# Performance work log

Hardware: AMD Instinct MI355X
Metric: run time of the kernel (lower is better)

## Reference

```python
import jax, jax.numpy as jnp
import numpy as np

B = 16384          # batch
N_SPARSE = 16      # single-id sparse features
N_VARLEN = 4       # variable-length sparse features
L = 50             # max sequence length per varlen feature
V = 1_000_000      # vocab per table
D = 1              # linear embedding dim (DeepCTR Linear uses dim=1)
INIT_STD = 1e-4
EPS = 1e-8


def setup_inputs() -> dict:
    key = jax.random.key(0)
    k1, k2, k3 = jax.random.split(key, 3)
    X = jax.random.randint(k1, (B, N_SPARSE + N_VARLEN * L), 0, V, dtype=jnp.int32)
    sparse_tables = jax.random.normal(k2, (N_SPARSE, V, D), dtype=jnp.float32) * INIT_STD
    varlen_tables = jax.random.normal(k3, (N_VARLEN, V, D), dtype=jnp.float32) * INIT_STD
    return {"X": X, "sparse_tables": sparse_tables, "varlen_tables": varlen_tables}


def reference(X, sparse_tables, varlen_tables):
    # --- single-id sparse lookups: one gather per table, vectorized over tables ---
    sparse_ids = X[:, :N_SPARSE]                                  # [B, Ns]
    f_idx = jnp.arange(N_SPARSE)[None, :]                          # [1, Ns]
    sparse_emb = sparse_tables[f_idx, sparse_ids]                  # [B, Ns, D]

    # --- varlen lookups + masked mean pooling (mask: id != 0, DeepCTR convention) ---
    varlen_ids = X[:, N_SPARSE:].reshape(B, N_VARLEN, L)           # [B, Nv, L]
    v_idx = jnp.arange(N_VARLEN)[None, :, None]                    # [1, Nv, 1]
    varlen_emb = varlen_tables[v_idx, varlen_ids]                  # [B, Nv, L, D]
    mask = (varlen_ids != 0).astype(varlen_emb.dtype)[..., None]   # [B, Nv, L, 1]
    summed = jnp.sum(varlen_emb * mask, axis=2)                    # [B, Nv, D]
    lengths = jnp.sum(mask, axis=2)                                # [B, Nv, 1]
    pooled = summed / (lengths + EPS)                              # [B, Nv, D]

    # --- concat and flatten, matching torch.flatten(concat_fun(...), start_dim=1) ---
    out = jnp.concatenate([sparse_emb, pooled], axis=1)            # [B, Ns+Nv, D]
    return out.reshape(B, -1)                                      # [B, (Ns+Nv)*D]
```

## Files before the change

### kernel.cpp

```cpp
#include <hip/hip_runtime.h>

#define B 16384
#define N_SPARSE 16
#define N_VARLEN 4
#define L 50
#define V 1000000
#define ROW (N_SPARSE + N_VARLEN * L)
#define OUT_W (N_SPARSE + N_VARLEN)
#define KLANES 8

#define VARLEN_BLOCKS 2048
#define SPARSE_BLOCKS 1024
#define NVEC 3
#define NID  7

typedef int v2i __attribute__((ext_vector_type(2)));

__global__ __launch_bounds__(256) void emb_gather_pool_kernel(
    const int* __restrict__ X,
    const float* __restrict__ sparse_tables,
    const float* __restrict__ varlen_tables,
    float* __restrict__ out)
{
    const int bid = blockIdx.x;
    const int t   = threadIdx.x;

    if (bid < VARLEN_BLOCKS) {
        const int xcd  = bid & 7;
        const int f    = xcd & 3;
        const int half = xcd >> 2;
        const int slot = bid >> 3;
        const int task = t >> 3;
        const int lane = t & (KLANES - 1);
        const int row  = half * (B / 2) + slot * 32 + task;

        const int*   ids = X + row * ROW + N_SPARSE + f * L;
        const float* tab = varlen_tables + (long)f * V;

        int id[NID];
        #pragma unroll
        for (int k = 0; k < NVEC; ++k) {
            const v2i w = __builtin_nontemporal_load(
                reinterpret_cast<const v2i*>(ids + 2 * lane + 16 * k));
            id[2 * k]     = w.x;
            id[2 * k + 1] = w.y;
        }
        id[6] = (lane < 2) ? __builtin_nontemporal_load(ids + 48 + lane) : 0;

        float v[NID];
        #pragma unroll
        for (int k = 0; k < 6; ++k) {
            v[k] = tab[id[k]];
        }
        v[6] = 0.0f;
        if (lane < 2) {
            v[6] = tab[id[6]];
        }

        float sum = 0.0f;
        float cnt = 0.0f;
        #pragma unroll
        for (int k = 0; k < NID; ++k) {
            const float m = (id[k] != 0) ? 1.0f : 0.0f;
            sum = fmaf(m, v[k], sum);
            cnt += m;
        }

        #pragma unroll
        for (int off = 1; off < KLANES; off <<= 1) {
            sum += __shfl_xor(sum, off);
            cnt += __shfl_xor(cnt, off);
        }

        if (lane == 0) {
            __builtin_nontemporal_store(sum / (cnt + 1e-8f),
                                        out + row * OUT_W + N_SPARSE + f);
        }
    } else {
        const int sb  = bid - VARLEN_BLOCKS;
        const int rl  = t >> 4;
        const int j   = t & 15;
        const int row = sb * 16 + rl;

        const int   id = __builtin_nontemporal_load(X + row * ROW + j);
        const float v  = __builtin_nontemporal_load(sparse_tables + (long)j * V + id);
        __builtin_nontemporal_store(v, out + row * OUT_W + j);
    }
}

extern "C" void kernel_launch(void* const* d_in, const int* in_sizes, int n_in,
                              void* d_out, int out_size, void* d_ws, size_t ws_size,
                              hipStream_t stream) {
    const int*   X             = (const int*)  d_in[0];
    const float* sparse_tables = (const float*)d_in[1];
    const float* varlen_tables = (const float*)d_in[2];
    float*       out           = (float*)d_out;

    const int grid  = VARLEN_BLOCKS + SPARSE_BLOCKS;
    const int block = 256;

    emb_gather_pool_kernel<<<grid, block, 0, stream>>>(X, sparse_tables, varlen_tables, out);
}
```

Before: 126.5 us.

## Prefetch varlen tables with a streaming warm-up kernel before the gather

Adds a warm_kernel that reads all four varlen embedding tables sequentially with vector loads, so they sit in the large last-level cache before the random gathers run. Its result goes to the workspace scaled near zero, only so the loads are not optimised away. The main kernel is reordered so the sparse-lookup blocks come first and the varlen blocks after, with the per-XCD feature mapping kept. The intent is to turn scattered HBM accesses into cache hits, at the cost of an extra launch and a full 16MB streaming read on every call.

New measurement: 129.4 us. 2.3% more time.

```diff
diff --git a/kernel.cpp b/kernel.cpp
--- a/kernel.cpp
+++ b/kernel.cpp
@@ -9,12 +9,36 @@
 #define OUT_W (N_SPARSE + N_VARLEN)
 #define KLANES 8
 
+#define SPARSE_BLOCKS 1024
 #define VARLEN_BLOCKS 2048
-#define SPARSE_BLOCKS 1024
-#define NVEC 3
-#define NID  7
+#define WARM_BLOCKS   2048
 
-typedef int v2i __attribute__((ext_vector_type(2)));
+typedef int   v2i __attribute__((ext_vector_type(2)));
+typedef float v4f __attribute__((ext_vector_type(4)));
+
+__global__ __launch_bounds__(256) void warm_kernel(
+    const float* __restrict__ varlen_tables,
+    float* __restrict__ ws)
+{
+    const int bid  = blockIdx.x;
+    const int t    = threadIdx.x;
+    const int xcd  = bid & 7;
+    const int f    = xcd & 3;
+    const int slot = bid >> 3;
+    const float* tab = varlen_tables + (long)f * V;
+
+    float acc = 0.0f;
+    const int base = slot * 4096 + t * 4;
+    #pragma unroll
+    for (int c = 0; c < 4; ++c) {
+        const int g = base + c * 1024;
+        if (g + 4 <= V) {
+            const v4f w = *reinterpret_cast<const v4f*>(tab + g);
+            acc += w.x + w.y + w.z + w.w;
+        }
+    }
+    ws[bid] = acc * 1e-30f;
+}
 
 __global__ __launch_bounds__(256) void emb_gather_pool_kernel(
     const int* __restrict__ X,
@@ -25,66 +49,67 @@
     const int bid = blockIdx.x;
     const int t   = threadIdx.x;
 
-    if (bid < VARLEN_BLOCKS) {
-        const int xcd  = bid & 7;
-        const int f    = xcd & 3;
-        const int half = xcd >> 2;
-        const int slot = bid >> 3;
-        const int task = t >> 3;
-        const int lane = t & (KLANES - 1);
-        const int row  = half * (B / 2) + slot * 32 + task;
-
-        const int*   ids = X + row * ROW + N_SPARSE + f * L;
-        const float* tab = varlen_tables + (long)f * V;
-
-        int id[NID];
-        #pragma unroll
-        for (int k = 0; k < NVEC; ++k) {
-            const v2i w = __builtin_nontemporal_load(
-                reinterpret_cast<const v2i*>(ids + 2 * lane + 16 * k));
-            id[2 * k]     = w.x;
-            id[2 * k + 1] = w.y;
-        }
-        id[6] = (lane < 2) ? __builtin_nontemporal_load(ids + 48 + lane) : 0;
-
-        float v[NID];
-        #pragma unroll
-        for (int k = 0; k < 6; ++k) {
-            v[k] = tab[id[k]];
-        }
-        v[6] = 0.0f;
-        if (lane < 2) {
-            v[6] = tab[id[6]];
-        }
-
-        float sum = 0.0f;
-        float cnt = 0.0f;
-        #pragma unroll
-        for (int k = 0; k < NID; ++k) {
-            const float m = (id[k] != 0) ? 1.0f : 0.0f;
-            sum = fmaf(m, v[k], sum);
-            cnt += m;
-        }
-
-        #pragma unroll
-        for (int off = 1; off < KLANES; off <<= 1) {
-            sum += __shfl_xor(sum, off);
-            cnt += __shfl_xor(cnt, off);
-        }
-
-        if (lane == 0) {
-            __builtin_nontemporal_store(sum / (cnt + 1e-8f),
-                                        out + row * OUT_W + N_SPARSE + f);
-        }
-    } else {
-        const int sb  = bid - VARLEN_BLOCKS;
+    if (bid < SPARSE_BLOCKS) {
         const int rl  = t >> 4;
         const int j   = t & 15;
-        const int row = sb * 16 + rl;
+        const int row = bid * 16 + rl;
 
         const int   id = __builtin_nontemporal_load(X + row * ROW + j);
         const float v  = __builtin_nontemporal_load(sparse_tables + (long)j * V + id);
         __builtin_nontemporal_store(v, out + row * OUT_W + j);
+        return;
+    }
+
+    const int vb   = bid - SPARSE_BLOCKS;
+    const int xcd  = bid & 7;
+    const int f    = xcd & 3;
+    const int half = xcd >> 2;
+    const int slot = vb >> 3;
+    const int task = t >> 3;
+    const int lane = t & (KLANES - 1);
+    const int row  = half * (B / 2) + slot * 32 + task;
+
+    const int*   ids = X + row * ROW + N_SPARSE + f * L;
+    const float* tab = varlen_tables + (long)f * V;
+
+    int id[7];
+    #pragma unroll
+    for (int k = 0; k < 3; ++k) {
+        const v2i w = __builtin_nontemporal_load(
+            reinterpret_cast<const v2i*>(ids + 2 * lane + 16 * k));
+        id[2 * k]     = w.x;
+        id[2 * k + 1] = w.y;
+    }
+    id[6] = (lane < 2) ? __builtin_nontemporal_load(ids + 48 + lane) : 0;
+
+    float v[7];
+    #pragma unroll
+    for (int k = 0; k < 6; ++k) {
+        v[k] = tab[id[k]];
+    }
+    v[6] = 0.0f;
+    if (lane < 2) {
+        v[6] = tab[id[6]];
+    }
+
+    float sum = 0.0f;
+    float cnt = 0.0f;
+    #pragma unroll
+    for (int k = 0; k < 7; ++k) {
+        const float m = (id[k] != 0) ? 1.0f : 0.0f;
+        sum = fmaf(m, v[k], sum);
+        cnt += m;
+    }
+
+    #pragma unroll
+    for (int off = 1; off < KLANES; off <<= 1) {
+        sum += __shfl_xor(sum, off);
+        cnt += __shfl_xor(cnt, off);
+    }
+
+    if (lane == 0) {
+        __builtin_nontemporal_store(sum / (cnt + 1e-8f),
+                                    out + row * OUT_W + N_SPARSE + f);
     }
 }
 
@@ -95,9 +120,10 @@
     const float* sparse_tables = (const float*)d_in[1];
     const float* varlen_tables = (const float*)d_in[2];
     float*       out           = (float*)d_out;
+    float*       ws            = (float*)d_ws;
 
-    const int grid  = VARLEN_BLOCKS + SPARSE_BLOCKS;
-    const int block = 256;
+    warm_kernel<<<WARM_BLOCKS, 256, 0, stream>>>(varlen_tables, ws);
 
-    emb_gather_pool_kernel<<<grid, block, 0, stream>>>(X, sparse_tables, varlen_tables, out);
+    const int grid = SPARSE_BLOCKS + VARLEN_BLOCKS;
+    emb_gather_pool_kernel<<<grid, 256, 0, stream>>>(X, sparse_tables, varlen_tables, out);
 }
```
